# Kernel optimization log

Hardware: AMD Instinct MI355X
Metric: run time of the kernel (lower is better)

Reference implementation:

```python
import jax, jax.numpy as jnp
import numpy as np

N_NODES = 2000
N_FEAT = 16
HID = 64
RNN_LAYERS = 2
OUT_WIN = 24
OUT_DIM = 1
N_Q = 3
LN_EPS = 1e-5


def _layernorm(x, g, b):
    mu = jnp.mean(x, axis=-1, keepdims=True)
    var = jnp.mean((x - mu) ** 2, axis=-1, keepdims=True)
    return (x - mu) * jax.lax.rsqrt(var + LN_EPS) * g + b


def setup_inputs() -> dict:
    key = jax.random.key(0)
    ks = jax.random.split(key, 24)
    B, S, N, F, H = 4, 96, N_NODES, N_FEAT, HID
    E = 16000
    inp = {}
    inp['x'] = jax.random.normal(ks[0], (B, S, N, F), dtype=jnp.float32)
    inp['edge_index'] = jax.random.randint(ks[1], (2, E), 0, N, dtype=jnp.int64)
    inp['edge_weight'] = jax.random.uniform(ks[2], (E,), dtype=jnp.float32)
    sc = 1.0 / np.sqrt(H)
    inp['W_gcn'] = jax.random.normal(ks[3], (H, F)) * (1.0 / np.sqrt(F))
    inp['b_gcn'] = jnp.zeros((H,))
    inp['Wq'] = jax.random.normal(ks[4], (H, H)) * sc
    inp['Wk'] = jax.random.normal(ks[5], (H, H)) * sc
    inp['Wv'] = jax.random.normal(ks[6], (H, H)) * sc
    inp['v_w'] = jax.random.normal(ks[7], (1, H)) * sc
    inp['v_b'] = jnp.zeros((1,))
    inp['ln1_g'] = jnp.ones((H,)); inp['ln1_b'] = jnp.zeros((H,))
    inp['gru_Wih'] = jax.random.normal(ks[8], (RNN_LAYERS, 3 * H, H)) * sc
    inp['gru_Whh'] = jax.random.normal(ks[9], (RNN_LAYERS, 3 * H, H)) * sc
    inp['gru_bih'] = jnp.zeros((RNN_LAYERS, 3 * H))
    inp['gru_bhh'] = jnp.zeros((RNN_LAYERS, 3 * H))
    inp['ln2_g'] = jnp.ones((H,)); inp['ln2_b'] = jnp.zeros((H,))
    inp['pre1_W'] = jax.random.normal(ks[10], (2 * H, H)) * sc
    inp['pre1_b'] = jnp.zeros((2 * H,))
    inp['pre2_W'] = jax.random.normal(ks[11], (N * H, 2 * H)) * (1.0 / np.sqrt(2 * H))
    inp['pre2_b'] = jnp.zeros((N * H,))
    inp['low_W'] = jax.random.normal(ks[12], (OUT_WIN * OUT_DIM, H)) * sc
    inp['low_b'] = jnp.zeros((OUT_WIN * OUT_DIM,))
    inp['inc_W'] = jax.random.normal(ks[13], (OUT_WIN * OUT_DIM * (N_Q - 1), H)) * sc
    inp['inc_b'] = jnp.zeros((OUT_WIN * OUT_DIM * (N_Q - 1),))
    return inp


def reference(x, edge_index, edge_weight, W_gcn, b_gcn, Wq, Wk, Wv, v_w, v_b,
              ln1_g, ln1_b, gru_Wih, gru_Whh, gru_bih, gru_bhh, ln2_g, ln2_b,
              pre1_W, pre1_b, pre2_W, pre2_b, low_W, low_b, inc_W, inc_b):
    B, S, N, F = x.shape
    H = W_gcn.shape[0]
    # ---- GCNConv (PyG semantics: add self-loops, symmetric normalization) ----
    # Graph is identical across batch/timesteps, so vectorize the per-timestep
    # loop into one batched gather/scatter.
    src, dst = edge_index[0], edge_index[1]
    loops = jnp.arange(N, dtype=edge_index.dtype)
    src_a = jnp.concatenate([src, loops])
    dst_a = jnp.concatenate([dst, loops])
    ew_a = jnp.concatenate([edge_weight, jnp.ones((N,), dtype=edge_weight.dtype)])
    deg = jax.ops.segment_sum(ew_a, dst_a, num_segments=N)
    dinv = jnp.where(deg > 0, deg ** -0.5, 0.0)
    coef = dinv[src_a] * ew_a * dinv[dst_a]  # (E+N,)
    xw = jnp.einsum('bsnf,hf->bsnh', x, W_gcn)  # linear (no bias yet)
    msg = xw[:, :, src_a, :] * coef[None, None, :, None]  # (B,S,E+N,H)
    h = jnp.zeros((B, S, N, H), dtype=xw.dtype).at[:, :, dst_a].add(msg)
    h = jax.nn.elu(h + b_gcn)  # dropout is identity in eval
    # ---- additive attention over all (t, node) positions ----
    keys = h.reshape(B, S * N, H)
    query = h[:, -1].mean(axis=1)  # (B,H)
    qp = query @ Wq.T  # (B,H)
    kp = keys @ Wk.T   # (B,SN,H)
    vp = keys @ Wv.T
    energy = jnp.tanh(qp[:, None, :] + kp)
    scores = energy @ v_w[0] + v_b[0]  # (B,SN)
    attn = jax.nn.softmax(scores, axis=1)
    context = jnp.einsum('bk,bkh->bh', attn, vp)
    context = _layernorm(context, ln1_g, ln1_b)
    # ---- GRU with seq_len=1, h0=0 (torch gate order: r,z,n) ----
    inp = context
    for l in range(gru_Wih.shape[0]):
        gi = inp @ gru_Wih[l].T + gru_bih[l]  # (B,3H)
        gh = gru_bhh[l]                        # h_prev = 0
        i_r, i_z, i_n = jnp.split(gi, 3, axis=-1)
        h_r, h_z, h_n = jnp.split(gh, 3, axis=-1)
        r = jax.nn.sigmoid(i_r + h_r)
        z = jax.nn.sigmoid(i_z + h_z)
        n = jnp.tanh(i_n + r * h_n)
        inp = (1.0 - z) * n  # + z * 0
    final = _layernorm(inp, ln2_g, ln2_b)
    # ---- pre_head -> per-node features ----
    f = jax.nn.elu(final @ pre1_W.T + pre1_b)
    nf = (f @ pre2_W.T + pre2_b).reshape(B, N, H)
    # ---- monotonic quantile head ----
    q_low = (nf @ low_W.T + low_b).reshape(B, N, OUT_WIN, OUT_DIM)
    inc = jax.nn.softplus((nf @ inc_W.T + inc_b).reshape(B, N, OUT_WIN, OUT_DIM, N_Q - 1))
    q1 = q_low + inc[..., 0]
    q2 = q1 + inc[..., 1]
    quant = jnp.stack([q_low, q1, q2], axis=-1)  # (B,N,OW,OD,Q)
    predictions = jnp.transpose(quant, (0, 2, 1, 3, 4))  # (B,OW,N,OD,Q)
    return predictions, attn.reshape(B, S, N)
```

## Files before the change

kernel.cpp:

```cpp
#include <hip/hip_runtime.h>

#define B 4
#define S 96
#define NN 2000
#define FF 16
#define HH 64
#define EE 16000
#define SN (S*NN)
#define SLICES (B*S)
#define BSN (B*SN)
#define KB_TOTAL (BSN/16)
#define KB_PER_B (SN/16)
#define OUT_PRED (B*24*NN*3)

typedef __attribute__((ext_vector_type(8))) short short8;
typedef __attribute__((ext_vector_type(4))) float f32x4;

__device__ __forceinline__ unsigned short f2bf(float f){
  unsigned u = __float_as_uint(f);
  u += 0x7fffu + ((u >> 16) & 1u);
  return (unsigned short)(u >> 16);
}
__device__ __forceinline__ float bf2f(unsigned short s){
  return __uint_as_float(((unsigned)s) << 16);
}
__device__ __forceinline__ float fast_tanh(float x){
  float e = __expf(2.0f * x);
  return 1.0f - 2.0f / (e + 1.0f);
}
__device__ __forceinline__ float sigm(float x){ return 1.0f / (1.0f + __expf(-x)); }
__device__ __forceinline__ float eluf(float x){ return x > 0.0f ? x : expm1f(x); }
__device__ __forceinline__ float softplusf_(float x){
  return fmaxf(x, 0.0f) + log1pf(__expf(-fabsf(x)));
}

__global__ void k_pinit(float* __restrict__ degw, int* __restrict__ cnt){
  int i = blockIdx.x * 256 + threadIdx.x;
  if (i < NN){ degw[i] = 1.0f; cnt[i] = 1; }
}

__global__ void k_deg(const int* __restrict__ ei, const float* __restrict__ ew,
                      float* __restrict__ degw, int* __restrict__ cnt){
  int e = blockIdx.x * 256 + threadIdx.x;
  if (e < EE){
    int d = ei[EE + e];
    atomicAdd(&degw[d], ew[e]);
    atomicAdd(&cnt[d], 1);
  }
}

__global__ void k_scan(const int* __restrict__ cnt, float* __restrict__ degw,
                       int* __restrict__ rowptr, int* __restrict__ curs){
  __shared__ int tsum[256];
  int tid = threadIdx.x;
  for (int i = tid; i < NN; i += 256){
    float deg = degw[i];
    degw[i] = deg > 0.0f ? rsqrtf(deg) : 0.0f;
  }
  int base = tid * 8;
  int loc[8]; int s = 0;
  #pragma unroll
  for (int j = 0; j < 8; ++j){
    int v = (base + j < NN) ? cnt[base + j] : 0;
    loc[j] = s; s += v;
  }
  tsum[tid] = s;
  __syncthreads();
  for (int off = 1; off < 256; off <<= 1){
    int v = (tid >= off) ? tsum[tid - off] : 0;
    __syncthreads();
    tsum[tid] += v;
    __syncthreads();
  }
  int excl = tsum[tid] - s;
  #pragma unroll
  for (int j = 0; j < 8; ++j)
    if (base + j < NN){ rowptr[base + j] = excl + loc[j]; curs[base + j] = excl + loc[j]; }
  if (tid == 0) rowptr[NN] = EE + NN;
}

__global__ void k_fill(const int* __restrict__ ei, const float* __restrict__ ew,
                       const float* __restrict__ dinv, int* __restrict__ curs,
                       uint2* __restrict__ epack){
  int e = blockIdx.x * 256 + threadIdx.x;
  if (e < EE){
    int s0 = ei[e], d = ei[EE + e];
    int pos = atomicAdd(&curs[d], 1);
    epack[pos] = make_uint2((unsigned)s0, __float_as_uint(dinv[s0] * ew[e] * dinv[d]));
  }
  int i = blockIdx.x * 256 + threadIdx.x;
  if (i < NN){
    int pos = atomicAdd(&curs[i], 1);
    epack[pos] = make_uint2((unsigned)i, __float_as_uint(dinv[i] * dinv[i]));
  }
}

__global__ __launch_bounds__(512) void k_agg(const float* __restrict__ x,
    const int* __restrict__ rowptr, const uint2* __restrict__ epack,
    unsigned* __restrict__ aggG){
  __shared__ unsigned xs[NN * 8];
  int tid = threadIdx.x;
  int slice = blockIdx.x;
  const float4* xg4 = (const float4*)(x + (size_t)slice * (NN * FF));
  for (int i = tid; i < 8000; i += 512){
    float4 v = xg4[i];
    int sl = i >> 2, q = i & 3;
    unsigned p0 = (unsigned)f2bf(v.x) | ((unsigned)f2bf(v.y) << 16);
    unsigned p1 = (unsigned)f2bf(v.z) | ((unsigned)f2bf(v.w) << 16);
    int j  = q >> 1;
    int jj = (j + (sl >> 1)) & 1;
    int base = sl * 8 + jj * 4 + (q & 1) * 2;
    xs[base] = p0; xs[base + 1] = p1;
  }
  __syncthreads();

  int rs[4], re[4];
  #pragma unroll
  for (int g = 0; g < 4; ++g){
    int n = g * 512 + tid;
    if (n < NN){ rs[g] = rowptr[n]; re[g] = rowptr[n + 1]; }
    else { rs[g] = 0; re[g] = 0; }
  }
  float agg[4][16];
  #pragma unroll
  for (int g = 0; g < 4; ++g)
    #pragma unroll
    for (int i = 0; i < 16; ++i) agg[g][i] = 0.0f;

  #pragma unroll
  for (int g = 0; g < 4; ++g){
    for (int e = rs[g]; e < re[g]; ++e){
      uint2 m = epack[e];
      int s = (int)m.x;
      float c = __uint_as_float(m.y);
      int r0 = ((s >> 1) & 1) * 4;
      uint4 ua = *(const uint4*)&xs[s * 8 + r0];
      uint4 ub = *(const uint4*)&xs[s * 8 + (r0 ^ 4)];
      agg[g][0]  += c * __uint_as_float(ua.x << 16);
      agg[g][1]  += c * __uint_as_float(ua.x & 0xffff0000u);
      agg[g][2]  += c * __uint_as_float(ua.y << 16);
      agg[g][3]  += c * __uint_as_float(ua.y & 0xffff0000u);
      agg[g][4]  += c * __uint_as_float(ua.z << 16);
      agg[g][5]  += c * __uint_as_float(ua.z & 0xffff0000u);
      agg[g][6]  += c * __uint_as_float(ua.w << 16);
      agg[g][7]  += c * __uint_as_float(ua.w & 0xffff0000u);
      agg[g][8]  += c * __uint_as_float(ub.x << 16);
      agg[g][9]  += c * __uint_as_float(ub.x & 0xffff0000u);
      agg[g][10] += c * __uint_as_float(ub.y << 16);
      agg[g][11] += c * __uint_as_float(ub.y & 0xffff0000u);
      agg[g][12] += c * __uint_as_float(ub.z << 16);
      agg[g][13] += c * __uint_as_float(ub.z & 0xffff0000u);
      agg[g][14] += c * __uint_as_float(ub.w << 16);
      agg[g][15] += c * __uint_as_float(ub.w & 0xffff0000u);
    }
  }
  #pragma unroll
  for (int g = 0; g < 4; ++g){
    int n = g * 512 + tid;
    if (n < NN){
      unsigned u[8];
      #pragma unroll
      for (int j = 0; j < 8; ++j)
        u[j] = (unsigned)f2bf(agg[g][2*j]) | ((unsigned)f2bf(agg[g][2*j+1]) << 16);
      uint4* dst = (uint4*)(aggG + ((size_t)slice * NN + n) * 8);
      dst[0] = make_uint4(u[0], u[1], u[2], u[3]);
      dst[1] = make_uint4(u[4], u[5], u[6], u[7]);
    }
  }
}

__global__ __launch_bounds__(256) void k_xform(const unsigned short* __restrict__ aggG,
    const float* __restrict__ Wg, const float* __restrict__ bg,
    unsigned short* __restrict__ h){
  int lane = threadIdx.x & 63;
  int wid  = threadIdx.x >> 6;
  int wgid = blockIdx.x * 4 + wid;
  int row16 = lane & 15, half = lane >> 4;

  short8 bf[4];
  #pragma unroll
  for (int t = 0; t < 4; ++t){
    short8 v;
    #pragma unroll
    for (int j = 0; j < 8; ++j) v[j] = 0;
    if (half < 2){
      const float* wr = Wg + (t * 16 + row16) * 16 + half * 8;
      #pragma unroll
      for (int j = 0; j < 8; ++j) v[j] = (short)f2bf(wr[j]);
    }
    bf[t] = v;
  }
  float bias[4];
  #pragma unroll
  for (int t = 0; t < 4; ++t) bias[t] = bg[t * 16 + row16];

  for (int nb = wgid; nb < KB_TOTAL; nb += 8192){
    short8 af;
    #pragma unroll
    for (int j = 0; j < 8; ++j) af[j] = 0;
    if (half < 2)
      af = *(const short8*)(aggG + ((size_t)nb * 16 + row16) * 16 + half * 8);

    f32x4 acc[4];
    #pragma unroll
    for (int t = 0; t < 4; ++t){
      f32x4 a = {0.f, 0.f, 0.f, 0.f};
      acc[t] = __builtin_amdgcn_mfma_f32_16x16x32_bf16(af, bf[t], a, 0, 0, 0);
    }
    unsigned short* hp = h + (size_t)nb * 16 * 64;
    #pragma unroll
    for (int t = 0; t < 4; ++t){
      #pragma unroll
      for (int r = 0; r < 4; ++r){
        float v = acc[t][r] + bias[t];
        float e = v > 0.0f ? v : __expf(v) - 1.0f;
        hp[(half * 4 + r) * 64 + t * 16 + row16] = f2bf(e);
      }
    }
  }
}

__global__ void k_query(const unsigned short* __restrict__ h,
                        const float* __restrict__ Wq, float* __restrict__ qp){
  __shared__ float part[256];
  __shared__ float q[64];
  int b = blockIdx.x, tid = threadIdx.x;
  int i = tid & 63, chunk = tid >> 6;
  const unsigned short* hb = h + ((size_t)(b * S + (S - 1)) * NN) * HH;
  float p = 0.0f;
  for (int n = chunk * 500; n < chunk * 500 + 500; ++n) p += bf2f(hb[n * HH + i]);
  part[tid] = p;
  __syncthreads();
  if (tid < 64) q[tid] = (part[tid] + part[tid+64] + part[tid+128] + part[tid+192]) * (1.0f / NN);
  __syncthreads();
  if (tid < 64){
    float acc = 0.0f;
    for (int k = 0; k < 64; ++k) acc += q[k] * Wq[tid * 64 + k];
    qp[b * 64 + tid] = acc;
  }
}

__global__ __launch_bounds__(256) void k_scores(const unsigned short* __restrict__ h,
    const float* __restrict__ Wk, const float* __restrict__ vw,
    const float* __restrict__ qp, float* __restrict__ scores){
  int lane = threadIdx.x & 63;
  int wid = threadIdx.x >> 6;
  int wgid = blockIdx.x * 4 + wid;
  int row16 = lane & 15, half = lane >> 4;

  short8 bf[4][2];
  #pragma unroll
  for (int t = 0; t < 4; ++t){
    int n = 16 * t + row16;
    #pragma unroll
    for (int s2 = 0; s2 < 2; ++s2){
      const float* wr = Wk + n * 64 + 32 * s2 + half * 8;
      short8 v;
      #pragma unroll
      for (int j = 0; j < 8; ++j) v[j] = (short)f2bf(wr[j]);
      bf[t][s2] = v;
    }
  }
  float vwv[4];
  #pragma unroll
  for (int t = 0; t < 4; ++t) vwv[t] = vw[16 * t + row16];

  for (int kb = wgid; kb < KB_TOTAL; kb += 8192){
    int b = kb / KB_PER_B;
    const short* hp = (const short*)h + (size_t)kb * 16 * 64;
    short8 af[2];
    #pragma unroll
    for (int s2 = 0; s2 < 2; ++s2)
      af[s2] = *(const short8*)(hp + row16 * 64 + 32 * s2 + half * 8);

    f32x4 acc[4];
    #pragma unroll
    for (int t = 0; t < 4; ++t){
      f32x4 a = {0.f, 0.f, 0.f, 0.f};
      a = __builtin_amdgcn_mfma_f32_16x16x32_bf16(af[0], bf[t][0], a, 0, 0, 0);
      a = __builtin_amdgcn_mfma_f32_16x16x32_bf16(af[1], bf[t][1], a, 0, 0, 0);
      acc[t] = a;
    }
    float part[4] = {0, 0, 0, 0};
    #pragma unroll
    for (int t = 0; t < 4; ++t){
      float qv = qp[b * 64 + 16 * t + row16];
      #pragma unroll
      for (int r = 0; r < 4; ++r)
        part[r] += vwv[t] * fast_tanh(qv + acc[t][r]);
    }
    #pragma unroll
    for (int r = 0; r < 4; ++r){
      part[r] += __shfl_xor(part[r], 1);
      part[r] += __shfl_xor(part[r], 2);
      part[r] += __shfl_xor(part[r], 4);
      part[r] += __shfl_xor(part[r], 8);
    }
    if (row16 == 0){
      #pragma unroll
      for (int r = 0; r < 4; ++r) scores[kb * 16 + half * 4 + r] = part[r];
    }
  }
}

__global__ void k_smax1(const float* __restrict__ scores, float* __restrict__ part2){
  __shared__ float red[256];
  int b = blockIdx.x >> 7, blk = blockIdx.x & 127, tid = threadIdx.x;
  const float* sc = scores + (size_t)b * SN + blk * 1500;
  float m = -1e30f;
  for (int k = tid; k < 1500; k += 256) m = fmaxf(m, sc[k]);
  red[tid] = m; __syncthreads();
  for (int s2 = 128; s2 > 0; s2 >>= 1){
    if (tid < s2) red[tid] = fmaxf(red[tid], red[tid + s2]);
    __syncthreads();
  }
  float bm = red[0]; __syncthreads();
  float sum = 0.f;
  for (int k = tid; k < 1500; k += 256) sum += __expf(sc[k] - bm);
  red[tid] = sum; __syncthreads();
  for (int s2 = 128; s2 > 0; s2 >>= 1){
    if (tid < s2) red[tid] += red[tid + s2];
    __syncthreads();
  }
  if (tid == 0){
    part2[(b * 128 + blk) * 2]     = bm;
    part2[(b * 128 + blk) * 2 + 1] = red[0];
  }
}

__global__ void k_smax2(const float* __restrict__ part2, float* __restrict__ Msum){
  int b = threadIdx.x;
  if (b < B){
    float M = -1e30f;
    for (int i = 0; i < 128; ++i) M = fmaxf(M, part2[(b * 128 + i) * 2]);
    float Ssum = 0.f;
    for (int i = 0; i < 128; ++i)
      Ssum += part2[(b * 128 + i) * 2 + 1] * __expf(part2[(b * 128 + i) * 2] - M);
    Msum[b] = M;
    Msum[4 + b] = 1.0f / Ssum;
  }
}

__global__ __launch_bounds__(256) void k_ctx(const float* __restrict__ scores,
    const float* __restrict__ Msum, const unsigned short* __restrict__ h,
    float* __restrict__ ctx_raw, float* __restrict__ outp){
  __shared__ float red[4 * 64];
  int lane = threadIdx.x & 63, wid = threadIdx.x >> 6;
  int b = blockIdx.x >> 7;
  int blk = blockIdx.x & 127;
  int kr = lane >> 3, fb = lane & 7;
  float M = Msum[b], Si = Msum[4 + b];
  const float* sc = scores + (size_t)b * SN;
  const unsigned short* hb = h + (size_t)b * SN * 64;
  float* ao = outp + OUT_PRED + (size_t)b * SN;

  float acc[8];
  #pragma unroll
  for (int j = 0; j < 8; ++j) acc[j] = 0.0f;

  for (int k0 = (blk * 4 + wid) * 8; k0 < SN; k0 += 4096){
    int k = k0 + kr;
    float a = __expf(sc[k] - M) * Si;
    uint4 u = *(const uint4*)(hb + (size_t)k * 64 + fb * 8);
    if (fb == 0) ao[k] = a;
    acc[0] += a * __uint_as_float(u.x << 16);
    acc[1] += a * __uint_as_float(u.x & 0xffff0000u);
    acc[2] += a * __uint_as_float(u.y << 16);
    acc[3] += a * __uint_as_float(u.y & 0xffff0000u);
    acc[4] += a * __uint_as_float(u.z << 16);
    acc[5] += a * __uint_as_float(u.z & 0xffff0000u);
    acc[6] += a * __uint_as_float(u.w << 16);
    acc[7] += a * __uint_as_float(u.w & 0xffff0000u);
  }
  #pragma unroll
  for (int j = 0; j < 8; ++j){
    acc[j] += __shfl_xor(acc[j], 8);
    acc[j] += __shfl_xor(acc[j], 16);
    acc[j] += __shfl_xor(acc[j], 32);
  }
  if (kr == 0){
    #pragma unroll
    for (int j = 0; j < 8; ++j) red[wid * 64 + fb * 8 + j] = acc[j];
  }
  __syncthreads();
  if (wid == 0){
    float t = red[lane] + red[64 + lane] + red[128 + lane] + red[192 + lane];
    atomicAdd(&ctx_raw[b * 64 + lane], t);
  }
}

__global__ void k_head(const float* __restrict__ ctx_raw, const float* __restrict__ Wv,
    const float* __restrict__ ln1g, const float* __restrict__ ln1b,
    const float* __restrict__ Wih, const float* __restrict__ bih,
    const float* __restrict__ bhh,
    const float* __restrict__ ln2g, const float* __restrict__ ln2b,
    const float* __restrict__ pre1W, const float* __restrict__ pre1b,
    float* __restrict__ fout){
  __shared__ float cr[64], vec[64], stat[2];
  int b = blockIdx.x, t = threadIdx.x;
  if (t < 64) cr[t] = ctx_raw[b * 64 + t];
  __syncthreads();
  float c = 0.f;
  if (t < 64){
    for (int i = 0; i < 64; ++i) c += cr[i] * Wv[t * 64 + i];
  }
  __syncthreads();
  if (t < 64) vec[t] = c;
  __syncthreads();
  if (t == 0){
    float mu = 0; for (int i = 0; i < 64; ++i) mu += vec[i]; mu *= (1.f/64.f);
    float va = 0; for (int i = 0; i < 64; ++i){ float d = vec[i] - mu; va += d * d; }
    va *= (1.f/64.f);
    stat[0] = mu; stat[1] = rsqrtf(va + 1e-5f);
  }
  __syncthreads();
  if (t < 64) cr[t] = (vec[t] - stat[0]) * stat[1] * ln1g[t] + ln1b[t];
  __syncthreads();
  for (int l = 0; l < 2; ++l){
    float nv = 0.f;
    if (t < 64){
      const float* W = Wih + l * 192 * 64;
      const float* bi = bih + l * 192;
      const float* bh = bhh + l * 192;
      float ir = bi[t], iz = bi[64 + t], in_ = bi[128 + t];
      for (int i = 0; i < 64; ++i){
        float v = cr[i];
        ir  += v * W[t * 64 + i];
        iz  += v * W[(64 + t) * 64 + i];
        in_ += v * W[(128 + t) * 64 + i];
      }
      float r = sigm(ir + bh[t]);
      float z = sigm(iz + bh[64 + t]);
      float nn2 = fast_tanh(in_ + r * bh[128 + t]);
      nv = (1.0f - z) * nn2;
    }
    __syncthreads();
    if (t < 64) cr[t] = nv;
    __syncthreads();
  }
  if (t == 0){
    float mu = 0; for (int i = 0; i < 64; ++i) mu += cr[i]; mu *= (1.f/64.f);
    float va = 0; for (int i = 0; i < 64; ++i){ float d = cr[i] - mu; va += d * d; }
    va *= (1.f/64.f);
    stat[0] = mu; stat[1] = rsqrtf(va + 1e-5f);
  }
  __syncthreads();
  if (t < 64) vec[t] = (cr[t] - stat[0]) * stat[1] * ln2g[t] + ln2b[t];
  __syncthreads();
  float fc = pre1b[t];
  for (int j = 0; j < 64; ++j) fc += vec[j] * pre1W[t * 64 + j];
  fout[b * 128 + t] = eluf(fc);
}

__global__ __launch_bounds__(256) void k_out(const float* __restrict__ f_g,
    const float* __restrict__ pre2W, const float* __restrict__ pre2b,
    const float* __restrict__ lowW, const float* __restrict__ lowb,
    const float* __restrict__ incW, const float* __restrict__ incb,
    float* __restrict__ outp){
  __shared__ float part[4 * 4 * 64];
  __shared__ float nf_lds[4 * 64];
  int lane = threadIdx.x & 63, w = threadIdx.x >> 6;
  int n = blockIdx.x;
  const float4* wr = (const float4*)(pre2W + ((size_t)(n * 64 + lane)) * 128 + w * 32);
  float a0 = 0, a1 = 0, a2 = 0, a3 = 0;
  #pragma unroll
  for (int c4 = 0; c4 < 8; ++c4){
    float4 wv4 = wr[c4];
    int cb = w * 32 + c4 * 4;
    a0 += wv4.x * f_g[cb]       + wv4.y * f_g[cb + 1]       + wv4.z * f_g[cb + 2]       + wv4.w * f_g[cb + 3];
    a1 += wv4.x * f_g[128 + cb] + wv4.y * f_g[128 + cb + 1] + wv4.z * f_g[128 + cb + 2] + wv4.w * f_g[128 + cb + 3];
    a2 += wv4.x * f_g[256 + cb] + wv4.y * f_g[256 + cb + 1] + wv4.z * f_g[256 + cb + 2] + wv4.w * f_g[256 + cb + 3];
    a3 += wv4.x * f_g[384 + cb] + wv4.y * f_g[384 + cb + 1] + wv4.z * f_g[384 + cb + 2] + wv4.w * f_g[384 + cb + 3];
  }
  part[(w * 4 + 0) * 64 + lane] = a0;
  part[(w * 4 + 1) * 64 + lane] = a1;
  part[(w * 4 + 2) * 64 + lane] = a2;
  part[(w * 4 + 3) * 64 + lane] = a3;
  __syncthreads();
  int b = w;
  float nf = pre2b[n * 64 + lane];
  #pragma unroll
  for (int w2 = 0; w2 < 4; ++w2) nf += part[(w2 * 4 + b) * 64 + lane];
  nf_lds[b * 64 + lane] = nf;
  __syncthreads();
  if (lane < 24){
    int wo = lane;
    float q0 = lowb[wo], i0 = incb[2 * wo], i1 = incb[2 * wo + 1];
    for (int j = 0; j < 64; ++j){
      float v = nf_lds[b * 64 + j];
      q0 += v * lowW[wo * 64 + j];
      i0 += v * incW[(2 * wo) * 64 + j];
      i1 += v * incW[(2 * wo + 1) * 64 + j];
    }
    float p0 = q0;
    float p1 = p0 + softplusf_(i0);
    float p2 = p1 + softplusf_(i1);
    size_t ob = ((size_t)(b * 24 + wo) * NN + n) * 3;
    outp[ob] = p0; outp[ob + 1] = p1; outp[ob + 2] = p2;
  }
}

extern "C" void kernel_launch(void* const* d_in, const int* in_sizes, int n_in,
                              void* d_out, int out_size, void* d_ws, size_t ws_size,
                              hipStream_t stream){
  const float* x     = (const float*)d_in[0];
  const int*   ei    = (const int*)d_in[1];
  const float* ew    = (const float*)d_in[2];
  const float* Wg    = (const float*)d_in[3];
  const float* bg    = (const float*)d_in[4];
  const float* Wq    = (const float*)d_in[5];
  const float* Wk    = (const float*)d_in[6];
  const float* Wv    = (const float*)d_in[7];
  const float* vw    = (const float*)d_in[8];
  const float* ln1g  = (const float*)d_in[10];
  const float* ln1b  = (const float*)d_in[11];
  const float* Wih   = (const float*)d_in[12];
  const float* bih   = (const float*)d_in[14];
  const float* bhh   = (const float*)d_in[15];
  const float* ln2g  = (const float*)d_in[16];
  const float* ln2b  = (const float*)d_in[17];
  const float* pre1W = (const float*)d_in[18];
  const float* pre1b = (const float*)d_in[19];
  const float* pre2W = (const float*)d_in[20];
  const float* pre2b = (const float*)d_in[21];
  const float* lowW  = (const float*)d_in[22];
  const float* lowb  = (const float*)d_in[23];
  const float* incW  = (const float*)d_in[24];
  const float* incb  = (const float*)d_in[25];
  float* outp = (float*)d_out;

  char* ws = (char*)d_ws;
  size_t off = 0;
  auto alloc = [&](size_t bytes) -> char* {
    char* p = ws + off;
    off += (bytes + 255) & ~(size_t)255;
    return p;
  };
  unsigned short* h  = (unsigned short*)alloc((size_t)BSN * 64 * 2);
  unsigned* aggG     = (unsigned*)alloc((size_t)BSN * 8 * 4);
  float* scores      = (float*)alloc((size_t)BSN * 4);
  int*   rowptr      = (int*)alloc((NN + 1) * 4);
  uint2* epack       = (uint2*)alloc((EE + NN) * 8);
  float* degw        = (float*)alloc(NN * 4);
  int*   cnt         = (int*)alloc(NN * 4);
  int*   curs        = (int*)alloc(NN * 4);
  float* qp          = (float*)alloc(B * 64 * 4);
  float* part2       = (float*)alloc(B * 128 * 2 * 4);
  float* Msum        = (float*)alloc(8 * 4);
  float* ctx_raw     = (float*)alloc(B * 64 * 4);
  float* f_g         = (float*)alloc(B * 128 * 4);
  (void)ws_size; (void)in_sizes; (void)n_in; (void)out_size;

  hipMemsetAsync(ctx_raw, 0, B * 64 * 4, stream);
  k_pinit <<<(NN + 255) / 256, 256, 0, stream>>>(degw, cnt);
  k_deg   <<<(EE + 255) / 256, 256, 0, stream>>>(ei, ew, degw, cnt);
  k_scan  <<<1, 256, 0, stream>>>(cnt, degw, rowptr, curs);
  k_fill  <<<(EE + 255) / 256, 256, 0, stream>>>(ei, ew, degw, curs, epack);
  k_agg   <<<SLICES, 512, 0, stream>>>(x, rowptr, epack, aggG);
  k_xform <<<2048, 256, 0, stream>>>((const unsigned short*)aggG, Wg, bg, h);
  k_query <<<B, 256, 0, stream>>>(h, Wq, qp);
  k_scores<<<2048, 256, 0, stream>>>(h, Wk, vw, qp, scores);
  k_smax1 <<<512, 256, 0, stream>>>(scores, part2);
  k_smax2 <<<1, 64, 0, stream>>>(part2, Msum);
  k_ctx   <<<512, 256, 0, stream>>>(scores, Msum, h, ctx_raw, outp);
  k_head  <<<B, 128, 0, stream>>>(ctx_raw, Wv, ln1g, ln1b, Wih, bih, bhh,
                                  ln2g, ln2b, pre1W, pre1b, f_g);
  k_out   <<<NN, 256, 0, stream>>>(f_g, pre2W, pre2b, lowW, lowb, incW, incb, outp);
}
```

Measured before the change: 246.6 us.

## Compute pre2 projection with bf16 MFMA and stage quantile weights in LDS

The output kernel now gives each wavefront one node, with four nodes per block and 500 blocks. The 64x128 pre2 matvec for the four batches runs as bf16 16x16x32 MFMA, with the f vectors packed as the B operand. The low and inc head weights are transposed into LDS once per block and reused across all four nodes, and the head loop is spread over lanes by (wo, batch). This cuts the scalar FMA work and the repeated global reads of the small head weights, at the cost of bf16 rounding on pre2W and f. It also wastes 12 of the 16 MFMA columns and makes each block do a 4.6K-element LDS fill.

```diff
diff --git a/kernel.cpp b/kernel.cpp
--- a/kernel.cpp
+++ b/kernel.cpp
@@ -457,46 +457,74 @@
     const float* __restrict__ lowW, const float* __restrict__ lowb,
     const float* __restrict__ incW, const float* __restrict__ incb,
     float* __restrict__ outp){
-  __shared__ float part[4 * 4 * 64];
-  __shared__ float nf_lds[4 * 64];
-  int lane = threadIdx.x & 63, w = threadIdx.x >> 6;
-  int n = blockIdx.x;
-  const float4* wr = (const float4*)(pre2W + ((size_t)(n * 64 + lane)) * 128 + w * 32);
-  float a0 = 0, a1 = 0, a2 = 0, a3 = 0;
-  #pragma unroll
-  for (int c4 = 0; c4 < 8; ++c4){
-    float4 wv4 = wr[c4];
-    int cb = w * 32 + c4 * 4;
-    a0 += wv4.x * f_g[cb]       + wv4.y * f_g[cb + 1]       + wv4.z * f_g[cb + 2]       + wv4.w * f_g[cb + 3];
-    a1 += wv4.x * f_g[128 + cb] + wv4.y * f_g[128 + cb + 1] + wv4.z * f_g[128 + cb + 2] + wv4.w * f_g[128 + cb + 3];
-    a2 += wv4.x * f_g[256 + cb] + wv4.y * f_g[256 + cb + 1] + wv4.z * f_g[256 + cb + 2] + wv4.w * f_g[256 + cb + 3];
-    a3 += wv4.x * f_g[384 + cb] + wv4.y * f_g[384 + cb + 1] + wv4.z * f_g[384 + cb + 2] + wv4.w * f_g[384 + cb + 3];
-  }
-  part[(w * 4 + 0) * 64 + lane] = a0;
-  part[(w * 4 + 1) * 64 + lane] = a1;
-  part[(w * 4 + 2) * 64 + lane] = a2;
-  part[(w * 4 + 3) * 64 + lane] = a3;
-  __syncthreads();
-  int b = w;
-  float nf = pre2b[n * 64 + lane];
-  #pragma unroll
-  for (int w2 = 0; w2 < 4; ++w2) nf += part[(w2 * 4 + b) * 64 + lane];
-  nf_lds[b * 64 + lane] = nf;
-  __syncthreads();
-  if (lane < 24){
-    int wo = lane;
-    float q0 = lowb[wo], i0 = incb[2 * wo], i1 = incb[2 * wo + 1];
-    for (int j = 0; j < 64; ++j){
-      float v = nf_lds[b * 64 + j];
-      q0 += v * lowW[wo * 64 + j];
-      i0 += v * incW[(2 * wo) * 64 + j];
-      i1 += v * incW[(2 * wo + 1) * 64 + j];
-    }
-    float p0 = q0;
-    float p1 = p0 + softplusf_(i0);
-    float p2 = p1 + softplusf_(i1);
-    size_t ob = ((size_t)(b * 24 + wo) * NN + n) * 3;
-    outp[ob] = p0; outp[ob + 1] = p1; outp[ob + 2] = p2;
+  __shared__ float w72T[64 * 72];
+  __shared__ float nf_lds[4][64 * 4];
+  int tid = threadIdx.x;
+  int lane = tid & 63, wid = tid >> 6;
+  int row16 = lane & 15, half = lane >> 4;
+
+  for (int i = tid; i < 64 * 72; i += 256){
+    int j = i / 72, o = i - j * 72;
+    w72T[i] = (o < 24) ? lowW[o * 64 + j] : incW[(o - 24) * 64 + j];
+  }
+
+  short8 bfr[4];
+  #pragma unroll
+  for (int s = 0; s < 4; ++s){
+    short8 v;
+    #pragma unroll
+    for (int j = 0; j < 8; ++j) v[j] = 0;
+    if (row16 < 4){
+      const float* fr = f_g + row16 * 128 + s * 32 + half * 8;
+      #pragma unroll
+      for (int j = 0; j < 8; ++j) v[j] = (short)f2bf(fr[j]);
+    }
+    bfr[s] = v;
+  }
+  __syncthreads();
+
+  int n = blockIdx.x * 4 + wid;
+  float* nfw = &nf_lds[wid][0];
+  #pragma unroll
+  for (int rb = 0; rb < 4; ++rb){
+    f32x4 acc = {0.f, 0.f, 0.f, 0.f};
+    #pragma unroll
+    for (int s = 0; s < 4; ++s){
+      const float* ar = pre2W + ((size_t)(n * 64 + rb * 16 + row16)) * 128 + s * 32 + half * 8;
+      short8 av;
+      #pragma unroll
+      for (int j = 0; j < 8; ++j) av[j] = (short)f2bf(ar[j]);
+      acc = __builtin_amdgcn_mfma_f32_16x16x32_bf16(av, bfr[s], acc, 0, 0, 0);
+    }
+    if (row16 < 4){
+      #pragma unroll
+      for (int r = 0; r < 4; ++r){
+        int j = rb * 16 + half * 4 + r;
+        nfw[j * 4 + row16] = acc[r] + pre2b[n * 64 + j];
+      }
+    }
+  }
+  __syncthreads();
+
+  #pragma unroll
+  for (int rnd = 0; rnd < 2; ++rnd){
+    int wo = rnd * 16 + (lane >> 2);
+    int b = lane & 3;
+    if (wo < 24){
+      float q0 = lowb[wo], i0 = incb[2 * wo], i1 = incb[2 * wo + 1];
+      #pragma unroll 4
+      for (int j = 0; j < 64; ++j){
+        float v = nfw[j * 4 + b];
+        q0 += v * w72T[j * 72 + wo];
+        i0 += v * w72T[j * 72 + 24 + 2 * wo];
+        i1 += v * w72T[j * 72 + 24 + 2 * wo + 1];
+      }
+      float p0 = q0;
+      float p1 = p0 + softplusf_(i0);
+      float p2 = p1 + softplusf_(i1);
+      size_t ob = ((size_t)(b * 24 + wo) * NN + n) * 3;
+      outp[ob] = p0; outp[ob + 1] = p1; outp[ob + 2] = p2;
+    }
   }
 }
 
@@ -565,5 +593,5 @@
   k_ctx   <<<512, 256, 0, stream>>>(scores, Msum, h, ctx_raw, outp);
   k_head  <<<B, 128, 0, stream>>>(ctx_raw, Wv, ln1g, ln1b, Wih, bih, bhh,
                                   ln2g, ln2b, pre1W, pre1b, f_g);
-  k_out   <<<NN, 256, 0, stream>>>(f_g, pre2W, pre2b, lowW, lowb, incW, incb, outp);
-}
+  k_out   <<<500, 256, 0, stream>>>(f_g, pre2W, pre2b, lowW, lowb, incW, incb, outp);
+}
```

After: 227.2 us. 7.9% less time.
